# Kernel optimization log

Hardware: AMD Instinct MI355X
Metric: run time of the kernel (lower is better)

## Reference

```python
import jax, jax.numpy as jnp
import numpy as np

NEG_SLOPE_GAT = 0.2   # GATConv internal LeakyReLU
NEG_SLOPE_ACT = 0.01  # nn.LeakyReLU default
BN_EPS = 1e-5


def leaky(x, s):
    return jnp.where(x >= 0, x, s * x)


def gat_conv(x, src, dst, ea, W, We, a_s, a_d, a_e, b, n):
    # PyG GATConv, heads=1, concat=True, add_self_loops=True, fill_value='mean'.
    # src/dst already include appended self loops; ea includes mean-filled loop attrs.
    h = x @ W                      # [N, 64]
    e = ea @ We                    # [E+N, 64]
    alpha_src = h @ a_s            # [N]
    alpha_dst = h @ a_d            # [N]
    logits = leaky(alpha_src[src] + alpha_dst[dst] + e @ a_e, NEG_SLOPE_GAT)
    m = jax.ops.segment_max(logits, dst, num_segments=n)
    ex = jnp.exp(logits - m[dst])
    denom = jax.ops.segment_sum(ex, dst, num_segments=n)  # >0 (self loops)
    coef = ex / denom[dst]
    out = jax.ops.segment_sum(h[src] * coef[:, None], dst, num_segments=n)
    return out + b


def batch_norm(x, g, b):
    mu = x.mean(0)
    var = x.var(0)
    return (x - mu) / jnp.sqrt(var + BN_EPS) * g + b


def setup_inputs() -> dict:
    key = jax.random.key(0)
    N, E, H = 100000, 1600000, 64
    ks = jax.random.split(key, 40)
    d = {}
    d["x"] = jax.random.normal(ks[0], (N, 2), jnp.float32)
    d["edge_attr"] = jax.random.normal(ks[1], (E, 2), jnp.float32)
    d["edge_index"] = jax.random.randint(ks[2], (2, E), 0, N, jnp.int32)
    d["mask"] = jax.random.randint(ks[3], (N,), 0, 2, jnp.int32)
    i = 4
    for name, din in (("gcn", 2), ("lit", 2), ("gcn2", 64), ("lit2", 64)):
        d[name + "_W"] = jax.random.normal(ks[i], (din, H), jnp.float32) * 0.1; i += 1
        d[name + "_We"] = jax.random.normal(ks[i], (2, H), jnp.float32) * 0.1; i += 1
        d[name + "_as"] = jax.random.normal(ks[i], (H,), jnp.float32) * 0.1; i += 1
        d[name + "_ad"] = jax.random.normal(ks[i], (H,), jnp.float32) * 0.1; i += 1
        d[name + "_ae"] = jax.random.normal(ks[i], (H,), jnp.float32) * 0.1; i += 1
        d[name + "_b"] = jnp.zeros((H,), jnp.float32)
    d["ln_g"] = jnp.ones((H,), jnp.float32)
    d["ln_beta"] = jnp.zeros((H,), jnp.float32)
    d["f1_W"] = jax.random.normal(ks[i], (H, 32), jnp.float32) * 0.1; i += 1
    d["f1_b"] = jnp.zeros((32,), jnp.float32)
    d["f2_W"] = jax.random.normal(ks[i], (32, 1), jnp.float32) * 0.1
    d["f2_b"] = jnp.zeros((1,), jnp.float32)
    return d


def reference(x, edge_attr, edge_index, mask,
              gcn_W, gcn_We, gcn_as, gcn_ad, gcn_ae, gcn_b,
              lit_W, lit_We, lit_as, lit_ad, lit_ae, lit_b,
              gcn2_W, gcn2_We, gcn2_as, gcn2_ad, gcn2_ae, gcn2_b,
              lit2_W, lit2_We, lit2_as, lit2_ad, lit2_ae, lit2_b,
              ln_g, ln_beta, f1_W, f1_b, f2_W, f2_b):
    n = x.shape[0]
    loop = jnp.arange(n, dtype=edge_index.dtype)
    src = jnp.concatenate([edge_index[0], loop])
    dst = jnp.concatenate([edge_index[1], loop])
    ea = jnp.concatenate([edge_attr,
                          jnp.broadcast_to(edge_attr.mean(0), (n, edge_attr.shape[1]))], 0)
    mf = mask.astype(x.dtype)[:, None]  # [N,1]

    h = gat_conv(x, src, dst, ea, lit_W, lit_We, lit_as, lit_ad, lit_ae, lit_b, n) * (1 - mf) \
      + gat_conv(x, src, dst, ea, gcn_W, gcn_We, gcn_as, gcn_ad, gcn_ae, gcn_b, n) * mf
    h = leaky(batch_norm(h, ln_g, ln_beta), NEG_SLOPE_ACT)

    h = gat_conv(h, src, dst, ea, lit2_W, lit2_We, lit2_as, lit2_ad, lit2_ae, lit2_b, n) * (1 - mf) \
      + gat_conv(h, src, dst, ea, gcn2_W, gcn2_We, gcn2_as, gcn2_ad, gcn2_ae, gcn2_b, n) * mf
    h = leaky(h, NEG_SLOPE_ACT)

    out = (leaky(h @ f1_W + f1_b, NEG_SLOPE_ACT) @ f2_W + f2_b)[:, 0]
    return out * mask.astype(out.dtype)
```

## Files before the change

### kernel.cpp

```cpp
#include <hip/hip_runtime.h>

#define NEG_GAT 0.2f
#define NEG_ACT 0.01f
#define BN_EPS 1e-5f

__device__ __forceinline__ float wred64(float v) {
  #pragma unroll
  for (int o = 32; o; o >>= 1) v += __shfl_down(v, o);
  return v;
}
__device__ __forceinline__ int wredi64(int v) {
  #pragma unroll
  for (int o = 32; o; o >>= 1) v += __shfl_down(v, o);
  return v;
}
__device__ __forceinline__ int wscani(int x, int lane) {
  #pragma unroll
  for (int off = 1; off < 64; off <<= 1) {
    int t = __shfl_up(x, off);
    if (lane >= off) x += t;
  }
  return x;
}

__global__ void k_prep(const float* WL1, const float* WeL1, const float* asL1,
                       const float* adL1, const float* aeL1,
                       const float* WG1, const float* WeG1, const float* asG1,
                       const float* adG1, const float* aeG1,
                       const float* WL2, const float* WeL2, const float* asL2,
                       const float* adL2, const float* aeL2,
                       const float* WG2, const float* WeG2, const float* asG2,
                       const float* adG2, const float* aeG2,
                       float* ae2, float* l1c, float* was2) {
  int lane = threadIdx.x;
  const float* We[4] = {WeL1, WeG1, WeL2, WeG2};
  const float* ae[4] = {aeL1, aeG1, aeL2, aeG2};
  for (int s = 0; s < 4; s++) {
    float v0 = wred64(We[s][lane] * ae[s][lane]);
    float v1 = wred64(We[s][64 + lane] * ae[s][lane]);
    if (lane == 0) { ae2[2 * s] = v0; ae2[2 * s + 1] = v1; }
  }
  const float* W1[2] = {WL1, WG1};
  const float* a1s[2] = {asL1, asG1};
  const float* a1d[2] = {adL1, adG1};
  for (int t = 0; t < 2; t++) {
    float ws0 = wred64(W1[t][lane] * a1s[t][lane]);
    float ws1 = wred64(W1[t][64 + lane] * a1s[t][lane]);
    float wd0 = wred64(W1[t][lane] * a1d[t][lane]);
    float wd1 = wred64(W1[t][64 + lane] * a1d[t][lane]);
    if (lane == 0) {
      l1c[4 * t + 0] = ws0; l1c[4 * t + 1] = ws1;
      l1c[4 * t + 2] = wd0; l1c[4 * t + 3] = wd1;
    }
  }
  const float* W2[2] = {WL2, WG2};
  const float* a2s[2] = {asL2, asG2};
  const float* a2d[2] = {adL2, adG2};
  for (int t = 0; t < 2; t++) {
    float ss = 0.f, sd = 0.f;
    for (int j = 0; j < 64; j++) {
      float w = W2[t][lane * 64 + j];
      ss += w * a2s[t][j];
      sd += w * a2d[t][j];
    }
    was2[(2 * t) * 64 + lane] = ss;
    was2[(2 * t + 1) * 64 + lane] = sd;
  }
}

__global__ void __launch_bounds__(256)
k_eamean(const float* __restrict__ eattr, float* acc, int E) {
  int i = blockIdx.x * blockDim.x + threadIdx.x;
  float s0 = 0.f, s1 = 0.f;
  for (int e = i; e < E; e += gridDim.x * blockDim.x) {
    float2 v = ((const float2*)eattr)[e];
    s0 += v.x; s1 += v.y;
  }
  s0 = wred64(s0);
  s1 = wred64(s1);
  if ((threadIdx.x & 63) == 0) {
    atomicAdd(&acc[0], s0);
    atomicAdd(&acc[1], s1);
  }
}

__global__ void __launch_bounds__(256)
k_hist(const int* __restrict__ ei, int* __restrict__ cnt, int E) {
  int e = blockIdx.x * blockDim.x + threadIdx.x;
  if (e < E) atomicAdd(&cnt[ei[E + e]], 1);
}

__global__ void __launch_bounds__(256)
k_scanA(const int* __restrict__ cnt, int* __restrict__ bsum, int N) {
  __shared__ int wsum[4];
  int tid = threadIdx.x, lane = tid & 63, wid = tid >> 6;
  int base = blockIdx.x * 1024 + tid * 4;
  int t = 0;
  if (base + 3 < N) {
    int4 q = *(const int4*)(cnt + base);
    t = q.x + q.y + q.z + q.w;
  } else {
    if (base < N) t += cnt[base];
    if (base + 1 < N) t += cnt[base + 1];
    if (base + 2 < N) t += cnt[base + 2];
    if (base + 3 < N) t += cnt[base + 3];
  }
  t = wredi64(t);
  if (lane == 0) wsum[wid] = t;
  __syncthreads();
  if (tid == 0) bsum[blockIdx.x] = wsum[0] + wsum[1] + wsum[2] + wsum[3];
}

__global__ void __launch_bounds__(1024)
k_scanB(int* __restrict__ bsum, int* __restrict__ offs, int nb, int E, int N) {
  __shared__ int wsum[16];
  int tid = threadIdx.x, lane = tid & 63, wid = tid >> 6;
  int v = (tid < nb) ? bsum[tid] : 0;
  int x = wscani(v, lane);
  if (lane == 63) wsum[wid] = x;
  __syncthreads();
  if (wid == 0) {
    int w = (lane < 16) ? wsum[lane] : 0;
    w = wscani(w, lane);
    if (lane < 16) wsum[lane] = w;
  }
  __syncthreads();
  int incl = x + (wid ? wsum[wid - 1] : 0);
  if (tid < nb) bsum[tid] = incl - v;
  if (tid == 0) offs[N] = E;
}

__global__ void __launch_bounds__(256)
k_scanC(const int* __restrict__ cnt, const int* __restrict__ bsum,
        int* __restrict__ offs, int* __restrict__ cur, int N) {
  __shared__ int wsum[4];
  int tid = threadIdx.x, lane = tid & 63, wid = tid >> 6;
  int base = blockIdx.x * 1024 + tid * 4;
  int v0 = 0, v1 = 0, v2 = 0, v3 = 0;
  if (base + 3 < N) {
    int4 q = *(const int4*)(cnt + base);
    v0 = q.x; v1 = q.y; v2 = q.z; v3 = q.w;
  } else {
    if (base < N) v0 = cnt[base];
    if (base + 1 < N) v1 = cnt[base + 1];
    if (base + 2 < N) v2 = cnt[base + 2];
    if (base + 3 < N) v3 = cnt[base + 3];
  }
  int t = v0 + v1 + v2 + v3;
  int incl = wscani(t, lane);
  int exclT = incl - t;
  if (lane == 63) wsum[wid] = incl;
  __syncthreads();
  int wb = 0;
  if (wid > 0) wb += wsum[0];
  if (wid > 1) wb += wsum[1];
  if (wid > 2) wb += wsum[2];
  int eb = bsum[blockIdx.x] + wb + exclT;
  if (base < N)     { offs[base] = eb;           cur[base] = eb; }
  if (base + 1 < N) { int u = eb + v0;           offs[base + 1] = u; cur[base + 1] = u; }
  if (base + 2 < N) { int u = eb + v0 + v1;      offs[base + 2] = u; cur[base + 2] = u; }
  if (base + 3 < N) { int u = eb + v0 + v1 + v2; offs[base + 3] = u; cur[base + 3] = u; }
}

__global__ void __launch_bounds__(256)
k_node1(const float* __restrict__ x,
        const float* __restrict__ WL, const float* __restrict__ WG,
        const float* __restrict__ l1c,
        float* __restrict__ hL, float* __restrict__ hG,
        float* asL, float* adL, float* asG, float* adG, int N) {
  int idx = blockIdx.x * blockDim.x + threadIdx.x;
  int n = idx >> 6, lane = idx & 63;
  if (n >= N) return;
  float2 xv = ((const float2*)x)[n];
  hL[(size_t)n * 64 + lane] = xv.x * WL[lane] + xv.y * WL[64 + lane];
  hG[(size_t)n * 64 + lane] = xv.x * WG[lane] + xv.y * WG[64 + lane];
  if (lane == 0) {
    asL[n] = xv.x * l1c[0] + xv.y * l1c[1];
    adL[n] = xv.x * l1c[2] + xv.y * l1c[3];
    asG[n] = xv.x * l1c[4] + xv.y * l1c[5];
    adG[n] = xv.x * l1c[6] + xv.y * l1c[7];
  }
}

__global__ void __launch_bounds__(256)
k_fill(const int* __restrict__ ei, const float* __restrict__ eattr,
       const int* __restrict__ mask, const float* __restrict__ ae2,
       const float* __restrict__ asL1, const float* __restrict__ asG1,
       int* __restrict__ cur, int4* __restrict__ edg, int E) {
  int e = blockIdx.x * blockDim.x + threadIdx.x;
  if (e >= E) return;
  int s = ei[e], d = ei[E + e];
  int m = mask[d];
  float2 ea = ((const float2*)eattr)[e];
  float as1 = m ? asG1[s] : asL1[s];
  float t1 = as1 + ea.x * (m ? ae2[2] : ae2[0]) + ea.y * (m ? ae2[3] : ae2[1]);
  float t2 =       ea.x * (m ? ae2[6] : ae2[4]) + ea.y * (m ? ae2[7] : ae2[5]);
  int j = atomicAdd(&cur[d], 1);
  edg[j] = make_int4(s, __float_as_int(t1), __float_as_int(t2), m);
}

__global__ void __launch_bounds__(256)
k_refill(const float* __restrict__ asL2, const float* __restrict__ asG2,
         int4* __restrict__ edg, int E) {
  int j = blockIdx.x * blockDim.x + threadIdx.x;
  if (j >= E) return;
  int4 v = edg[j];
  float as2 = (v.w ? asG2 : asL2)[v.x];
  edg[j].y = __float_as_int(as2 + __int_as_float(v.z));
}

__device__ __forceinline__ float4 gat_row4(
    int n, int lane, int m,
    const int* __restrict__ offs, const int4* __restrict__ edg,
    const float* __restrict__ hL, const float* __restrict__ hG,
    const float* __restrict__ asL, const float* __restrict__ adL,
    const float* __restrict__ asG, const float* __restrict__ adG,
    const float* __restrict__ ae2, const float* __restrict__ eacc, float invE) {
  const float* as_p = m ? asG : asL;
  const float4* h4  = (const float4*)(m ? hG : hL);
  float ad = (m ? adG : adL)[n];
  float k0 = m ? ae2[2] : ae2[0];
  float k1 = m ? ae2[3] : ae2[1];
  int sub = lane & 15, grp = lane >> 4;
  float lg = as_p[n] + ad + (eacc[0] * invE) * k0 + (eacc[1] * invE) * k1;
  lg = lg >= 0.f ? lg : NEG_GAT * lg;
  float exs = __expf(lg);
  float4 hs = h4[(size_t)n * 16 + sub];
  float w = (grp == 0) ? exs : 0.f;
  float ax = w * hs.x, ay = w * hs.y, az = w * hs.z, aw = w * hs.w;
  float denom = w;
  int j = offs[n], end = offs[n + 1];
  for (; j < end; j += 8) {
    int i0 = j + grp, i1 = j + 4 + grp;
    int c0 = i0 < end ? i0 : end - 1;
    int c1 = i1 < end ? i1 : end - 1;
    int4 r0 = edg[(size_t)c0];
    int4 r1 = edg[(size_t)c1];
    float4 h0 = h4[(size_t)r0.x * 16 + sub];
    float4 h1 = h4[(size_t)r1.x * 16 + sub];
    float l0 = __int_as_float(r0.y) + ad;
    float l1 = __int_as_float(r1.y) + ad;
    l0 = l0 >= 0.f ? l0 : NEG_GAT * l0;
    l1 = l1 >= 0.f ? l1 : NEG_GAT * l1;
    float e0 = (i0 < end) ? __expf(l0) : 0.f;
    float e1 = (i1 < end) ? __expf(l1) : 0.f;
    denom += e0 + e1;
    ax = fmaf(e0, h0.x, ax); ay = fmaf(e0, h0.y, ay);
    az = fmaf(e0, h0.z, az); aw = fmaf(e0, h0.w, aw);
    ax = fmaf(e1, h1.x, ax); ay = fmaf(e1, h1.y, ay);
    az = fmaf(e1, h1.z, az); aw = fmaf(e1, h1.w, aw);
  }
  #pragma unroll
  for (int off = 16; off < 64; off <<= 1) {
    ax += __shfl_xor(ax, off); ay += __shfl_xor(ay, off);
    az += __shfl_xor(az, off); aw += __shfl_xor(aw, off);
    denom += __shfl_xor(denom, off);
  }
  float inv = 1.f / denom;
  return make_float4(ax * inv, ay * inv, az * inv, aw * inv);
}

__global__ void __launch_bounds__(256)
k_gat1(const int* __restrict__ offs, const int4* __restrict__ edg,
       const int* __restrict__ mask,
       const float* __restrict__ hL, const float* __restrict__ hG,
       const float* __restrict__ asL, const float* __restrict__ adL,
       const float* __restrict__ asG, const float* __restrict__ adG,
       const float* __restrict__ ae2, const float* __restrict__ eacc,
       float invE, const float* __restrict__ bL,
       const float* __restrict__ bG, float* __restrict__ C, int N) {
  int idx = blockIdx.x * blockDim.x + threadIdx.x;
  int n = idx >> 6, lane = idx & 63;
  if (n >= N) return;
  int m = mask[n];
  float4 o = gat_row4(n, lane, m, offs, edg, hL, hG,
                      asL, adL, asG, adG, ae2, eacc, invE);
  if (lane < 16) {
    float4 b4 = ((const float4*)(m ? bG : bL))[lane];
    o.x += b4.x; o.y += b4.y; o.z += b4.z; o.w += b4.w;
    ((float4*)C)[(size_t)n * 16 + lane] = o;
  }
}

__global__ void __launch_bounds__(256)
k_bnstat(const float* __restrict__ C, float* sums, float* sq, int N) {
  __shared__ float ls[256], lq[256];
  int col = threadIdx.x & 63, rg = threadIdx.x >> 6;
  float s = 0.f, q = 0.f;
  for (int r = blockIdx.x * 4 + rg; r < N; r += gridDim.x * 4) {
    float v = C[(size_t)r * 64 + col];
    s += v; q += v * v;
  }
  ls[threadIdx.x] = s; lq[threadIdx.x] = q;
  __syncthreads();
  if (rg == 0) {
    s = ls[col] + ls[col + 64] + ls[col + 128] + ls[col + 192];
    q = lq[col] + lq[col + 64] + lq[col + 128] + lq[col + 192];
    atomicAdd(&sums[col], s);
    atomicAdd(&sq[col], q);
  }
}

__global__ void __launch_bounds__(256)
k_node2(const float* __restrict__ C,
        const float* __restrict__ sums, const float* __restrict__ sq,
        const float* __restrict__ g, const float* __restrict__ beta,
        const float* __restrict__ WL, const float* __restrict__ WG,
        const float* __restrict__ was2,
        float* __restrict__ hL, float* __restrict__ hG,
        float* asL, float* adL, float* asG, float* adG, int N) {
  int idx = blockIdx.x * blockDim.x + threadIdx.x;
  int n = idx >> 6, lane = idx & 63;
  if (n >= N) return;
  float invN = 1.0f / (float)N;
  float mu = sums[lane] * invN;
  float var = sq[lane] * invN - mu * mu;
  float v = C[(size_t)n * 64 + lane];
  v = (v - mu) * rsqrtf(var + BN_EPS) * g[lane] + beta[lane];
  float c = v >= 0.f ? v : NEG_ACT * v;
  float d0 = wred64(c * was2[lane]);
  float d1 = wred64(c * was2[64 + lane]);
  float d2 = wred64(c * was2[128 + lane]);
  float d3 = wred64(c * was2[192 + lane]);
  if (lane == 0) { asL[n] = d0; adL[n] = d1; asG[n] = d2; adG[n] = d3; }
  float accL = 0.f, accG = 0.f;
  #pragma unroll
  for (int k = 0; k < 64; k++) {
    float cb = __shfl(c, k);
    accL += cb * WL[k * 64 + lane];
    accG += cb * WG[k * 64 + lane];
  }
  hL[(size_t)n * 64 + lane] = accL;
  hG[(size_t)n * 64 + lane] = accG;
}

__global__ void __launch_bounds__(256)
k_gat2_mlp(const int* __restrict__ offs, const int4* __restrict__ edg,
           const int* __restrict__ mask,
           const float* __restrict__ hL, const float* __restrict__ hG,
           const float* __restrict__ asL, const float* __restrict__ adL,
           const float* __restrict__ asG, const float* __restrict__ adG,
           const float* __restrict__ ae2, const float* __restrict__ eacc,
           float invE, const float* __restrict__ bL,
           const float* __restrict__ bG,
           const float* __restrict__ f1W, const float* __restrict__ f1b,
           const float* __restrict__ f2W, const float* __restrict__ f2b,
           float* __restrict__ out, int N) {
  int idx = blockIdx.x * blockDim.x + threadIdx.x;
  int n = idx >> 6, lane = idx & 63;
  if (n >= N) return;
  int m = mask[n];
  float4 o = gat_row4(n, lane, m, offs, edg, hL, hG,
                      asL, adL, asG, adG, ae2, eacc, invE);
  float4 b4 = ((const float4*)(m ? bG : bL))[lane & 15];
  float cv[4];
  cv[0] = o.x + b4.x; cv[1] = o.y + b4.y;
  cv[2] = o.z + b4.z; cv[3] = o.w + b4.w;
  #pragma unroll
  for (int q = 0; q < 4; q++)
    cv[q] = cv[q] >= 0.f ? cv[q] : NEG_ACT * cv[q];
  float acc = 0.f;
  #pragma unroll
  for (int k = 0; k < 64; k++) {
    float cb = __shfl(cv[k & 3], k >> 2);
    if (lane < 32) acc = fmaf(cb, f1W[k * 32 + lane], acc);
  }
  float p = 0.f;
  if (lane < 32) {
    float t = acc + f1b[lane];
    t = t >= 0.f ? t : NEG_ACT * t;
    p = t * f2W[lane];
  }
  p = wred64(p);
  if (lane == 0) out[n] = (p + f2b[0]) * (float)m;
}

extern "C" void kernel_launch(void* const* d_in, const int* in_sizes, int n_in,
                              void* d_out, int out_size, void* d_ws, size_t ws_size,
                              hipStream_t stream) {
  const float* x     = (const float*)d_in[0];
  const float* eattr = (const float*)d_in[1];
  const int*   ei    = (const int*)d_in[2];
  const int*   mask  = (const int*)d_in[3];
  const float* gcn_W  = (const float*)d_in[4];
  const float* gcn_We = (const float*)d_in[5];
  const float* gcn_as = (const float*)d_in[6];
  const float* gcn_ad = (const float*)d_in[7];
  const float* gcn_ae = (const float*)d_in[8];
  const float* gcn_b  = (const float*)d_in[9];
  const float* lit_W  = (const float*)d_in[10];
  const float* lit_We = (const float*)d_in[11];
  const float* lit_as = (const float*)d_in[12];
  const float* lit_ad = (const float*)d_in[13];
  const float* lit_ae = (const float*)d_in[14];
  const float* lit_b  = (const float*)d_in[15];
  const float* gcn2_W  = (const float*)d_in[16];
  const float* gcn2_We = (const float*)d_in[17];
  const float* gcn2_as = (const float*)d_in[18];
  const float* gcn2_ad = (const float*)d_in[19];
  const float* gcn2_ae = (const float*)d_in[20];
  const float* gcn2_b  = (const float*)d_in[21];
  const float* lit2_W  = (const float*)d_in[22];
  const float* lit2_We = (const float*)d_in[23];
  const float* lit2_as = (const float*)d_in[24];
  const float* lit2_ad = (const float*)d_in[25];
  const float* lit2_ae = (const float*)d_in[26];
  const float* lit2_b  = (const float*)d_in[27];
  const float* ln_g    = (const float*)d_in[28];
  const float* ln_beta = (const float*)d_in[29];
  const float* f1W = (const float*)d_in[30];
  const float* f1b = (const float*)d_in[31];
  const float* f2W = (const float*)d_in[32];
  const float* f2b = (const float*)d_in[33];

  const int N = in_sizes[3];
  const int E = in_sizes[1] / 2;
  const size_t N64 = (size_t)N * 64;

  int4*  edg   = (int4*)d_ws;
  float* C     = (float*)(edg + E);
  float* A     = C + N64;
  float* B     = A + N64;
  int*   cnt   = (int*)(B + N64);
  float* sums  = (float*)(cnt + N);
  float* sq    = sums + 64;
  float* eacc  = sq + 64;
  float* ae2   = eacc + 2;
  float* l1c   = ae2 + 8;
  float* was2  = l1c + 8;
  int*   offs  = (int*)(was2 + 256);
  int*   cur   = offs + N + 1;
  int*   bsum  = cur + N;
  float* asL   = (float*)(bsum + 1024);
  float* adL   = asL + N;
  float* asG   = adL + N;
  float* adG   = asG + N;

  const float invE = 1.0f / (float)E;
  const int TB = 256;
  const int nodeBlocks = (int)((N64 + TB - 1) / TB);
  const int eBlocks = (E + TB - 1) / TB;
  const int nb = (N + 1023) / 1024;

  hipMemsetAsync(cnt, 0, ((size_t)N + 130) * sizeof(float), stream);

  k_prep<<<1, 64, 0, stream>>>(lit_W, lit_We, lit_as, lit_ad, lit_ae,
                               gcn_W, gcn_We, gcn_as, gcn_ad, gcn_ae,
                               lit2_W, lit2_We, lit2_as, lit2_ad, lit2_ae,
                               gcn2_W, gcn2_We, gcn2_as, gcn2_ad, gcn2_ae,
                               ae2, l1c, was2);
  k_eamean<<<1024, TB, 0, stream>>>(eattr, eacc, E);
  k_hist<<<eBlocks, TB, 0, stream>>>(ei, cnt, E);
  k_scanA<<<nb, TB, 0, stream>>>(cnt, bsum, N);
  k_scanB<<<1, 1024, 0, stream>>>(bsum, offs, nb, E, N);
  k_scanC<<<nb, TB, 0, stream>>>(cnt, bsum, offs, cur, N);
  k_node1<<<nodeBlocks, TB, 0, stream>>>(x, lit_W, gcn_W, l1c,
                                         A, B, asL, adL, asG, adG, N);
  k_fill<<<eBlocks, TB, 0, stream>>>(ei, eattr, mask, ae2, asL, asG,
                                     cur, edg, E);
  k_gat1<<<nodeBlocks, TB, 0, stream>>>(offs, edg, mask, A, B,
                                        asL, adL, asG, adG, ae2, eacc, invE,
                                        lit_b, gcn_b, C, N);
  k_bnstat<<<384, TB, 0, stream>>>(C, sums, sq, N);
  k_node2<<<nodeBlocks, TB, 0, stream>>>(C, sums, sq, ln_g, ln_beta,
                                         lit2_W, gcn2_W, was2,
                                         A, B, asL, adL, asG, adG, N);
  k_refill<<<eBlocks, TB, 0, stream>>>(asL, asG, edg, E);
  k_gat2_mlp<<<nodeBlocks, TB, 0, stream>>>(offs, edg, mask, A, B,
                                            asL, adL, asG, adG, ae2 + 4, eacc, invE,
                                            lit2_b, gcn2_b, f1W, f1b, f2W, f2b,
                                            (float*)d_out, N);
}
```

Before: 865.8 us.

## Aggregate before projecting in both GAT layers to shrink gathered rows

Uses linearity of attention aggregation to gather low-dimensional inputs instead of projected 64-wide features. Layer 1 stores source x (2 floats) plus the logit in a float4 edge record, aggregates it with one lane per edge, then applies W. Layer 2 gathers the normalized 64-wide activations C and applies the 64x64 weight after aggregation, fused into the MLP kernel. This removes k_node1 and the hL/hG projection buffers and cuts layer-1 gather traffic sharply. The cost is an extra edge array written in k_fill, and the per-node matmul moves into the gather kernel.

```diff
diff --git a/kernel.cpp b/kernel.cpp
--- a/kernel.cpp
+++ b/kernel.cpp
@@ -163,123 +163,70 @@
 }
 
 __global__ void __launch_bounds__(256)
-k_node1(const float* __restrict__ x,
-        const float* __restrict__ WL, const float* __restrict__ WG,
-        const float* __restrict__ l1c,
-        float* __restrict__ hL, float* __restrict__ hG,
-        float* asL, float* adL, float* asG, float* adG, int N) {
-  int idx = blockIdx.x * blockDim.x + threadIdx.x;
-  int n = idx >> 6, lane = idx & 63;
-  if (n >= N) return;
-  float2 xv = ((const float2*)x)[n];
-  hL[(size_t)n * 64 + lane] = xv.x * WL[lane] + xv.y * WL[64 + lane];
-  hG[(size_t)n * 64 + lane] = xv.x * WG[lane] + xv.y * WG[64 + lane];
-  if (lane == 0) {
-    asL[n] = xv.x * l1c[0] + xv.y * l1c[1];
-    adL[n] = xv.x * l1c[2] + xv.y * l1c[3];
-    asG[n] = xv.x * l1c[4] + xv.y * l1c[5];
-    adG[n] = xv.x * l1c[6] + xv.y * l1c[7];
-  }
-}
-
-__global__ void __launch_bounds__(256)
 k_fill(const int* __restrict__ ei, const float* __restrict__ eattr,
-       const int* __restrict__ mask, const float* __restrict__ ae2,
-       const float* __restrict__ asL1, const float* __restrict__ asG1,
-       int* __restrict__ cur, int4* __restrict__ edg, int E) {
+       const float* __restrict__ x, const int* __restrict__ mask,
+       const float* __restrict__ ae2, const float* __restrict__ l1c,
+       int* __restrict__ cur, float4* __restrict__ edg1,
+       int4* __restrict__ edg2, int E) {
   int e = blockIdx.x * blockDim.x + threadIdx.x;
   if (e >= E) return;
   int s = ei[e], d = ei[E + e];
   int m = mask[d];
   float2 ea = ((const float2*)eattr)[e];
-  float as1 = m ? asG1[s] : asL1[s];
-  float t1 = as1 + ea.x * (m ? ae2[2] : ae2[0]) + ea.y * (m ? ae2[3] : ae2[1]);
-  float t2 =       ea.x * (m ? ae2[6] : ae2[4]) + ea.y * (m ? ae2[7] : ae2[5]);
+  float2 xs = ((const float2*)x)[s];
+  const float* lc = l1c + 4 * m;
+  float t1 = xs.x * lc[0] + xs.y * lc[1]
+           + ea.x * (m ? ae2[2] : ae2[0]) + ea.y * (m ? ae2[3] : ae2[1]);
+  float t2 = ea.x * (m ? ae2[6] : ae2[4]) + ea.y * (m ? ae2[7] : ae2[5]);
   int j = atomicAdd(&cur[d], 1);
-  edg[j] = make_int4(s, __float_as_int(t1), __float_as_int(t2), m);
-}
-
-__global__ void __launch_bounds__(256)
-k_refill(const float* __restrict__ asL2, const float* __restrict__ asG2,
-         int4* __restrict__ edg, int E) {
-  int j = blockIdx.x * blockDim.x + threadIdx.x;
-  if (j >= E) return;
-  int4 v = edg[j];
-  float as2 = (v.w ? asG2 : asL2)[v.x];
-  edg[j].y = __float_as_int(as2 + __int_as_float(v.z));
-}
-
-__device__ __forceinline__ float4 gat_row4(
-    int n, int lane, int m,
-    const int* __restrict__ offs, const int4* __restrict__ edg,
-    const float* __restrict__ hL, const float* __restrict__ hG,
-    const float* __restrict__ asL, const float* __restrict__ adL,
-    const float* __restrict__ asG, const float* __restrict__ adG,
-    const float* __restrict__ ae2, const float* __restrict__ eacc, float invE) {
-  const float* as_p = m ? asG : asL;
-  const float4* h4  = (const float4*)(m ? hG : hL);
-  float ad = (m ? adG : adL)[n];
-  float k0 = m ? ae2[2] : ae2[0];
-  float k1 = m ? ae2[3] : ae2[1];
-  int sub = lane & 15, grp = lane >> 4;
-  float lg = as_p[n] + ad + (eacc[0] * invE) * k0 + (eacc[1] * invE) * k1;
-  lg = lg >= 0.f ? lg : NEG_GAT * lg;
-  float exs = __expf(lg);
-  float4 hs = h4[(size_t)n * 16 + sub];
-  float w = (grp == 0) ? exs : 0.f;
-  float ax = w * hs.x, ay = w * hs.y, az = w * hs.z, aw = w * hs.w;
-  float denom = w;
-  int j = offs[n], end = offs[n + 1];
-  for (; j < end; j += 8) {
-    int i0 = j + grp, i1 = j + 4 + grp;
-    int c0 = i0 < end ? i0 : end - 1;
-    int c1 = i1 < end ? i1 : end - 1;
-    int4 r0 = edg[(size_t)c0];
-    int4 r1 = edg[(size_t)c1];
-    float4 h0 = h4[(size_t)r0.x * 16 + sub];
-    float4 h1 = h4[(size_t)r1.x * 16 + sub];
-    float l0 = __int_as_float(r0.y) + ad;
-    float l1 = __int_as_float(r1.y) + ad;
-    l0 = l0 >= 0.f ? l0 : NEG_GAT * l0;
-    l1 = l1 >= 0.f ? l1 : NEG_GAT * l1;
-    float e0 = (i0 < end) ? __expf(l0) : 0.f;
-    float e1 = (i1 < end) ? __expf(l1) : 0.f;
-    denom += e0 + e1;
-    ax = fmaf(e0, h0.x, ax); ay = fmaf(e0, h0.y, ay);
-    az = fmaf(e0, h0.z, az); aw = fmaf(e0, h0.w, aw);
-    ax = fmaf(e1, h1.x, ax); ay = fmaf(e1, h1.y, ay);
-    az = fmaf(e1, h1.z, az); aw = fmaf(e1, h1.w, aw);
-  }
-  #pragma unroll
-  for (int off = 16; off < 64; off <<= 1) {
-    ax += __shfl_xor(ax, off); ay += __shfl_xor(ay, off);
-    az += __shfl_xor(az, off); aw += __shfl_xor(aw, off);
-    denom += __shfl_xor(denom, off);
-  }
-  float inv = 1.f / denom;
-  return make_float4(ax * inv, ay * inv, az * inv, aw * inv);
-}
-
-__global__ void __launch_bounds__(256)
-k_gat1(const int* __restrict__ offs, const int4* __restrict__ edg,
-       const int* __restrict__ mask,
-       const float* __restrict__ hL, const float* __restrict__ hG,
-       const float* __restrict__ asL, const float* __restrict__ adL,
-       const float* __restrict__ asG, const float* __restrict__ adG,
-       const float* __restrict__ ae2, const float* __restrict__ eacc,
-       float invE, const float* __restrict__ bL,
-       const float* __restrict__ bG, float* __restrict__ C, int N) {
+  edg1[j] = make_float4(xs.x, xs.y, t1, 0.f);
+  edg2[j] = make_int4(s, 0, __float_as_int(t2), m);
+}
+
+__global__ void __launch_bounds__(256)
+k_gat1(const int* __restrict__ offs, const float4* __restrict__ edg1,
+       const float* __restrict__ x, const int* __restrict__ mask,
+       const float* __restrict__ l1c, const float* __restrict__ ae2,
+       const float* __restrict__ eacc, float invE,
+       const float* __restrict__ WL, const float* __restrict__ WG,
+       const float* __restrict__ bL, const float* __restrict__ bG,
+       float* __restrict__ C, int N) {
   int idx = blockIdx.x * blockDim.x + threadIdx.x;
   int n = idx >> 6, lane = idx & 63;
   if (n >= N) return;
   int m = mask[n];
-  float4 o = gat_row4(n, lane, m, offs, edg, hL, hG,
-                      asL, adL, asG, adG, ae2, eacc, invE);
-  if (lane < 16) {
-    float4 b4 = ((const float4*)(m ? bG : bL))[lane];
-    o.x += b4.x; o.y += b4.y; o.z += b4.z; o.w += b4.w;
-    ((float4*)C)[(size_t)n * 16 + lane] = o;
-  }
+  float2 xd = ((const float2*)x)[n];
+  const float* lc = l1c + 4 * m;
+  float as1 = xd.x * lc[0] + xd.y * lc[1];
+  float ad  = xd.x * lc[2] + xd.y * lc[3];
+  float k0 = m ? ae2[2] : ae2[0];
+  float k1 = m ? ae2[3] : ae2[1];
+  float lg = as1 + ad + (eacc[0] * invE) * k0 + (eacc[1] * invE) * k1;
+  lg = lg >= 0.f ? lg : NEG_GAT * lg;
+  float es = __expf(lg);
+  float y0 = 0.f, y1 = 0.f, den = 0.f;
+  int beg = offs[n], end = offs[n + 1];
+  for (int j = beg + lane; j < end; j += 64) {
+    float4 r = edg1[j];
+    float l = r.z + ad;
+    l = l >= 0.f ? l : NEG_GAT * l;
+    float e = __expf(l);
+    y0 = fmaf(e, r.x, y0);
+    y1 = fmaf(e, r.y, y1);
+    den += e;
+  }
+  #pragma unroll
+  for (int o = 1; o < 64; o <<= 1) {
+    y0 += __shfl_xor(y0, o);
+    y1 += __shfl_xor(y1, o);
+    den += __shfl_xor(den, o);
+  }
+  y0 += es * xd.x; y1 += es * xd.y; den += es;
+  float inv = 1.f / den;
+  const float* W = m ? WG : WL;
+  float outv = (y0 * W[lane] + y1 * W[64 + lane]) * inv
+             + (m ? bG : bL)[lane];
+  C[(size_t)n * 64 + lane] = outv;
 }
 
 __global__ void __launch_bounds__(256)
@@ -302,12 +249,10 @@
 }
 
 __global__ void __launch_bounds__(256)
-k_node2(const float* __restrict__ C,
+k_bnact(float* __restrict__ C,
         const float* __restrict__ sums, const float* __restrict__ sq,
         const float* __restrict__ g, const float* __restrict__ beta,
-        const float* __restrict__ WL, const float* __restrict__ WG,
         const float* __restrict__ was2,
-        float* __restrict__ hL, float* __restrict__ hG,
         float* asL, float* adL, float* asG, float* adG, int N) {
   int idx = blockIdx.x * blockDim.x + threadIdx.x;
   int n = idx >> 6, lane = idx & 63;
@@ -323,26 +268,78 @@
   float d2 = wred64(c * was2[128 + lane]);
   float d3 = wred64(c * was2[192 + lane]);
   if (lane == 0) { asL[n] = d0; adL[n] = d1; asG[n] = d2; adG[n] = d3; }
-  float accL = 0.f, accG = 0.f;
-  #pragma unroll
-  for (int k = 0; k < 64; k++) {
-    float cb = __shfl(c, k);
-    accL += cb * WL[k * 64 + lane];
-    accG += cb * WG[k * 64 + lane];
-  }
-  hL[(size_t)n * 64 + lane] = accL;
-  hG[(size_t)n * 64 + lane] = accG;
+  C[(size_t)n * 64 + lane] = c;
+}
+
+__global__ void __launch_bounds__(256)
+k_refill(const float* __restrict__ asL2, const float* __restrict__ asG2,
+         int4* __restrict__ edg, int E) {
+  int j = blockIdx.x * blockDim.x + threadIdx.x;
+  if (j >= E) return;
+  int4 v = edg[j];
+  float as2 = (v.w ? asG2 : asL2)[v.x];
+  edg[j].y = __float_as_int(as2 + __int_as_float(v.z));
+}
+
+__device__ __forceinline__ float4 agg_row4(
+    int n, int lane, int m,
+    const int* __restrict__ offs, const int4* __restrict__ edg,
+    const float4* __restrict__ c4,
+    const float* __restrict__ asL, const float* __restrict__ adL,
+    const float* __restrict__ asG, const float* __restrict__ adG,
+    const float* __restrict__ ae2, const float* __restrict__ eacc, float invE) {
+  float as_s = (m ? asG : asL)[n];
+  float ad   = (m ? adG : adL)[n];
+  float k0 = m ? ae2[2] : ae2[0];
+  float k1 = m ? ae2[3] : ae2[1];
+  int sub = lane & 15, grp = lane >> 4;
+  float lg = as_s + ad + (eacc[0] * invE) * k0 + (eacc[1] * invE) * k1;
+  lg = lg >= 0.f ? lg : NEG_GAT * lg;
+  float exs = __expf(lg);
+  float4 hs = c4[(size_t)n * 16 + sub];
+  float w = (grp == 0) ? exs : 0.f;
+  float ax = w * hs.x, ay = w * hs.y, az = w * hs.z, aw = w * hs.w;
+  float denom = w;
+  int j = offs[n], end = offs[n + 1];
+  for (; j < end; j += 8) {
+    int i0 = j + grp, i1 = j + 4 + grp;
+    int c0 = i0 < end ? i0 : end - 1;
+    int c1 = i1 < end ? i1 : end - 1;
+    int4 r0 = edg[(size_t)c0];
+    int4 r1 = edg[(size_t)c1];
+    float4 h0 = c4[(size_t)r0.x * 16 + sub];
+    float4 h1 = c4[(size_t)r1.x * 16 + sub];
+    float l0 = __int_as_float(r0.y) + ad;
+    float l1 = __int_as_float(r1.y) + ad;
+    l0 = l0 >= 0.f ? l0 : NEG_GAT * l0;
+    l1 = l1 >= 0.f ? l1 : NEG_GAT * l1;
+    float e0 = (i0 < end) ? __expf(l0) : 0.f;
+    float e1 = (i1 < end) ? __expf(l1) : 0.f;
+    denom += e0 + e1;
+    ax = fmaf(e0, h0.x, ax); ay = fmaf(e0, h0.y, ay);
+    az = fmaf(e0, h0.z, az); aw = fmaf(e0, h0.w, aw);
+    ax = fmaf(e1, h1.x, ax); ay = fmaf(e1, h1.y, ay);
+    az = fmaf(e1, h1.z, az); aw = fmaf(e1, h1.w, aw);
+  }
+  #pragma unroll
+  for (int off = 16; off < 64; off <<= 1) {
+    ax += __shfl_xor(ax, off); ay += __shfl_xor(ay, off);
+    az += __shfl_xor(az, off); aw += __shfl_xor(aw, off);
+    denom += __shfl_xor(denom, off);
+  }
+  float inv = 1.f / denom;
+  return make_float4(ax * inv, ay * inv, az * inv, aw * inv);
 }
 
 __global__ void __launch_bounds__(256)
 k_gat2_mlp(const int* __restrict__ offs, const int4* __restrict__ edg,
-           const int* __restrict__ mask,
-           const float* __restrict__ hL, const float* __restrict__ hG,
+           const int* __restrict__ mask, const float* __restrict__ C,
            const float* __restrict__ asL, const float* __restrict__ adL,
            const float* __restrict__ asG, const float* __restrict__ adG,
            const float* __restrict__ ae2, const float* __restrict__ eacc,
-           float invE, const float* __restrict__ bL,
-           const float* __restrict__ bG,
+           float invE,
+           const float* __restrict__ WL2, const float* __restrict__ WG2,
+           const float* __restrict__ bL, const float* __restrict__ bG,
            const float* __restrict__ f1W, const float* __restrict__ f1b,
            const float* __restrict__ f2W, const float* __restrict__ f2b,
            float* __restrict__ out, int N) {
@@ -350,19 +347,22 @@
   int n = idx >> 6, lane = idx & 63;
   if (n >= N) return;
   int m = mask[n];
-  float4 o = gat_row4(n, lane, m, offs, edg, hL, hG,
+  float4 o = agg_row4(n, lane, m, offs, edg, (const float4*)C,
                       asL, adL, asG, adG, ae2, eacc, invE);
-  float4 b4 = ((const float4*)(m ? bG : bL))[lane & 15];
-  float cv[4];
-  cv[0] = o.x + b4.x; cv[1] = o.y + b4.y;
-  cv[2] = o.z + b4.z; cv[3] = o.w + b4.w;
-  #pragma unroll
-  for (int q = 0; q < 4; q++)
-    cv[q] = cv[q] >= 0.f ? cv[q] : NEG_ACT * cv[q];
+  const float* W2 = m ? WG2 : WL2;
+  float cv[4] = {o.x, o.y, o.z, o.w};
+  float h2 = 0.f;
+  #pragma unroll
+  for (int k = 0; k < 64; k++) {
+    float yb = __shfl(cv[k & 3], k >> 2);
+    h2 = fmaf(yb, W2[k * 64 + lane], h2);
+  }
+  float c = h2 + (m ? bG : bL)[lane];
+  c = c >= 0.f ? c : NEG_ACT * c;
   float acc = 0.f;
   #pragma unroll
   for (int k = 0; k < 64; k++) {
-    float cb = __shfl(cv[k & 3], k >> 2);
+    float cb = __shfl(c, k);
     if (lane < 32) acc = fmaf(cb, f1W[k * 32 + lane], acc);
   }
   float p = 0.f;
@@ -417,24 +417,23 @@
   const int E = in_sizes[1] / 2;
   const size_t N64 = (size_t)N * 64;
 
-  int4*  edg   = (int4*)d_ws;
-  float* C     = (float*)(edg + E);
-  float* A     = C + N64;
-  float* B     = A + N64;
-  int*   cnt   = (int*)(B + N64);
-  float* sums  = (float*)(cnt + N);
-  float* sq    = sums + 64;
-  float* eacc  = sq + 64;
-  float* ae2   = eacc + 2;
-  float* l1c   = ae2 + 8;
-  float* was2  = l1c + 8;
-  int*   offs  = (int*)(was2 + 256);
-  int*   cur   = offs + N + 1;
-  int*   bsum  = cur + N;
-  float* asL   = (float*)(bsum + 1024);
-  float* adL   = asL + N;
-  float* asG   = adL + N;
-  float* adG   = asG + N;
+  float4* edg1 = (float4*)d_ws;
+  int4*   edg2 = (int4*)(edg1 + E);
+  float*  C    = (float*)(edg2 + E);
+  int*    cnt  = (int*)(C + N64);
+  float*  sums = (float*)(cnt + N);
+  float*  sq   = sums + 64;
+  float*  eacc = sq + 64;
+  float*  ae2  = eacc + 2;
+  float*  l1c  = ae2 + 8;
+  float*  was2 = l1c + 8;
+  int*    offs = (int*)(was2 + 256);
+  int*    cur  = offs + N + 1;
+  int*    bsum = cur + N;
+  float*  asL2 = (float*)(bsum + 1024);
+  float*  adL2 = asL2 + N;
+  float*  asG2 = adL2 + N;
+  float*  adG2 = asG2 + N;
 
   const float invE = 1.0f / (float)E;
   const int TB = 256;
@@ -454,20 +453,19 @@
   k_scanA<<<nb, TB, 0, stream>>>(cnt, bsum, N);
   k_scanB<<<1, 1024, 0, stream>>>(bsum, offs, nb, E, N);
   k_scanC<<<nb, TB, 0, stream>>>(cnt, bsum, offs, cur, N);
-  k_node1<<<nodeBlocks, TB, 0, stream>>>(x, lit_W, gcn_W, l1c,
-                                         A, B, asL, adL, asG, adG, N);
-  k_fill<<<eBlocks, TB, 0, stream>>>(ei, eattr, mask, ae2, asL, asG,
-                                     cur, edg, E);
-  k_gat1<<<nodeBlocks, TB, 0, stream>>>(offs, edg, mask, A, B,
-                                        asL, adL, asG, adG, ae2, eacc, invE,
+  k_fill<<<eBlocks, TB, 0, stream>>>(ei, eattr, x, mask, ae2, l1c,
+                                     cur, edg1, edg2, E);
+  k_gat1<<<nodeBlocks, TB, 0, stream>>>(offs, edg1, x, mask, l1c, ae2,
+                                        eacc, invE, lit_W, gcn_W,
                                         lit_b, gcn_b, C, N);
   k_bnstat<<<384, TB, 0, stream>>>(C, sums, sq, N);
-  k_node2<<<nodeBlocks, TB, 0, stream>>>(C, sums, sq, ln_g, ln_beta,
-                                         lit2_W, gcn2_W, was2,
-                                         A, B, asL, adL, asG, adG, N);
-  k_refill<<<eBlocks, TB, 0, stream>>>(asL, asG, edg, E);
-  k_gat2_mlp<<<nodeBlocks, TB, 0, stream>>>(offs, edg, mask, A, B,
-                                            asL, adL, asG, adG, ae2 + 4, eacc, invE,
-                                            lit2_b, gcn2_b, f1W, f1b, f2W, f2b,
+  k_bnact<<<nodeBlocks, TB, 0, stream>>>(C, sums, sq, ln_g, ln_beta, was2,
+                                         asL2, adL2, asG2, adG2, N);
+  k_refill<<<eBlocks, TB, 0, stream>>>(asL2, asG2, edg2, E);
+  k_gat2_mlp<<<nodeBlocks, TB, 0, stream>>>(offs, edg2, mask, C,
+                                            asL2, adL2, asG2, adG2,
+                                            ae2 + 4, eacc, invE,
+                                            lit2_W, gcn2_W, lit2_b, gcn2_b,
+                                            f1W, f1b, f2W, f2b,
                                             (float*)d_out, N);
 }
```

New measurement: 741.3 us. 1.17x faster.
